# Optimization experiments

Hardware: AMD Instinct MI355X
Metric: run time of the kernel (lower is better)

The kernel has to match this reference:

```python
import jax, jax.numpy as jnp
import numpy as np

DIM = 64
WIDTH = 128
INPUT_DIM = 16
N_NODES = 50000
N_EDGES = 100000
N_GRAPHS = 2500
STEPS = 5


def setup_inputs() -> dict:
    key = jax.random.key(0)
    ks = jax.random.split(key, 24)
    d = DIM
    def nrm(i, shape, fan_in):
        return jax.random.normal(ks[i], shape, jnp.float32) / np.float32(np.sqrt(fan_in))
    return {
        "x": jax.random.normal(ks[0], (N_NODES, INPUT_DIM - 1), jnp.float32),
        "z": jax.random.normal(ks[1], (N_NODES,), jnp.float32),
        "edge_attr": jax.random.uniform(ks[2], (N_EDGES, 5), jnp.float32),
        "lin0_w": nrm(3, (INPUT_DIM, d), INPUT_DIM),
        "lin0_b": jnp.zeros((d,), jnp.float32),
        "emlp_w1": nrm(4, (5, WIDTH), 5),
        "emlp_b1": jnp.zeros((WIDTH,), jnp.float32),
        "emlp_w2": nrm(5, (WIDTH, d * d), WIDTH),
        "emlp_b2": jnp.zeros((d * d,), jnp.float32),
        "conv_root": nrm(6, (d, d), d),
        "conv_bias": jnp.zeros((d,), jnp.float32),
        "gru_wi": nrm(7, (3 * d, d), d),
        "gru_wh": nrm(8, (3 * d, d), d),
        "gru_bi": jnp.zeros((3 * d,), jnp.float32),
        "gru_bh": jnp.zeros((3 * d,), jnp.float32),
        "lstm_wi": nrm(9, (4 * d, 2 * d), 2 * d),
        "lstm_wh": nrm(10, (4 * d, d), d),
        "lstm_bi": jnp.zeros((4 * d,), jnp.float32),
        "lstm_bh": jnp.zeros((4 * d,), jnp.float32),
        "lin1_w": nrm(11, (2 * d, d), 2 * d),
        "lin1_b": jnp.zeros((d,), jnp.float32),
        "lin2_w": nrm(12, (d, 1), d),
        "lin2_b": jnp.zeros((1,), jnp.float32),
        "edge_index": jax.random.randint(ks[13], (2, N_EDGES), 0, N_NODES),
        "batch": jnp.sort(jax.random.randint(ks[14], (N_NODES,), 0, N_GRAPHS)),
        "num_graphs": N_GRAPHS,
    }


def reference(x, z, edge_attr, lin0_w, lin0_b, emlp_w1, emlp_b1, emlp_w2, emlp_b2,
              conv_root, conv_bias, gru_wi, gru_wh, gru_bi, gru_bh,
              lstm_wi, lstm_wh, lstm_bi, lstm_bh, lin1_w, lin1_b, lin2_w, lin2_b,
              edge_index, batch, num_graphs):
    d = lin0_w.shape[1]
    n = x.shape[0]
    src, dst = edge_index[0], edge_index[1]
    # lin0 on [x | z]
    out = jax.nn.relu(jnp.concatenate([x, z[:, None]], axis=-1) @ lin0_w + lin0_b)  # [N, d]
    h = out
    # edge MLP -> per-edge weight matrix [E, d, d] (edge_attr fixed, compute once)
    ew = (jax.nn.relu(edge_attr @ emlp_w1 + emlp_b1) @ emlp_w2 + emlp_b2).reshape(-1, d, d)
    deg = jax.ops.segment_sum(jnp.ones_like(src, jnp.float32), dst, num_segments=n)
    denom = jnp.maximum(deg, 1.0)[:, None]
    for _ in range(STEPS):
        # NNConv: gather-matmul-scatter(mean) + root transform + bias
        msg = jnp.einsum('ei,eio->eo', out[src], ew)  # [E, d]
        aggr = jax.ops.segment_sum(msg, dst, num_segments=n) / denom
        m = jax.nn.relu(aggr + out @ conv_root + conv_bias)
        # GRU cell (torch gate order r, z, n)
        gi = m @ gru_wi.T + gru_bi
        gh = h @ gru_wh.T + gru_bh
        i_r, i_z, i_n = jnp.split(gi, 3, axis=-1)
        h_r, h_z, h_n = jnp.split(gh, 3, axis=-1)
        r = jax.nn.sigmoid(i_r + h_r)
        zg = jax.nn.sigmoid(i_z + h_z)
        ng = jnp.tanh(i_n + r * h_n)
        h = (1.0 - zg) * ng + zg * h
        out = h
    # Set2Set pooling (LSTM(2d -> d), torch gate order i, f, g, o)
    B = num_graphs
    q_star = jnp.zeros((B, 2 * d), out.dtype)
    hh = jnp.zeros((B, d), out.dtype)
    cc = jnp.zeros((B, d), out.dtype)
    for _ in range(STEPS):
        g = q_star @ lstm_wi.T + lstm_bi + hh @ lstm_wh.T + lstm_bh
        gi_, gf_, gg_, go_ = jnp.split(g, 4, axis=-1)
        cc = jax.nn.sigmoid(gf_) * cc + jax.nn.sigmoid(gi_) * jnp.tanh(gg_)
        hh = jax.nn.sigmoid(go_) * jnp.tanh(cc)
        q = hh
        e = jnp.sum(out * q[batch], axis=-1)  # [N]
        emax = jax.ops.segment_max(e, batch, num_segments=B)
        a = jnp.exp(e - emax[batch])
        asum = jax.ops.segment_sum(a, batch, num_segments=B) + 1e-16
        a = a / asum[batch]
        r_pool = jax.ops.segment_sum(a[:, None] * out, batch, num_segments=B)  # [B, d]
        q_star = jnp.concatenate([q, r_pool], axis=-1)
    y = jax.nn.relu(q_star @ lin1_w + lin1_b) @ lin2_w + lin2_b
    return y.reshape(-1)
```

## Files before the change

kernel.cpp:

```cpp
#include <hip/hip_runtime.h>
#include <hip/hip_bf16.h>

#define NN 50000
#define NE 100000
#define NG 2500
#define WW 128
#define EPAD 100096
#define KCH 264

typedef _Float16 h8 __attribute__((ext_vector_type(8)));
typedef _Float16 h4 __attribute__((ext_vector_type(4)));
typedef float    f4 __attribute__((ext_vector_type(4)));

#define GLOAD_LDS16(g, l) __builtin_amdgcn_global_load_lds( \
    (const __attribute__((address_space(1))) void*)(g),     \
    (__attribute__((address_space(3))) void*)(l), 16, 0, 0)

__device__ __forceinline__ float sigf(float x) { return 1.0f / (1.0f + __expf(-x)); }

__global__ void k_zero4(float4* __restrict__ p, int n4) {
    int i = blockIdx.x * 256 + threadIdx.x;
    if (i < n4) p[i] = make_float4(0.f, 0.f, 0.f, 0.f);
}

__global__ void k_transpose(float* dst, const float* src, int rows, int cols) {
    int idx = blockIdx.x * 256 + threadIdx.x;
    if (idx >= rows * cols) return;
    int r = idx / cols, c = idx % cols;
    dst[c * rows + r] = src[idx];
}

__global__ void k_lin0(const float* __restrict__ x, const float* __restrict__ z,
                       const float* __restrict__ w, const float* __restrict__ b,
                       float* __restrict__ s, _Float16* __restrict__ s16) {
    int idx = blockIdx.x * 256 + threadIdx.x;
    int n = idx >> 6, o = idx & 63;
    float acc = b[o];
#pragma unroll
    for (int i = 0; i < 15; i++) acc += x[n * 15 + i] * w[i * 64 + o];
    acc += z[n] * w[15 * 64 + o];
    float r = fmaxf(acc, 0.0f);
    s[idx] = r;
    s16[idx] = (_Float16)r;
}

__global__ void k_deg(const int* __restrict__ dstI, float* __restrict__ deg) {
    int e = blockIdx.x * 256 + threadIdx.x;
    if (e < NE) atomicAdd(&deg[dstI[e]], 1.0f);
}

__global__ void k_gstart(const int* __restrict__ batch, int* __restrict__ gstart) {
    int n = blockIdx.x * 256 + threadIdx.x;
    if (n > NN) return;
    int b1 = (n < NN) ? batch[n] : NG;
    int b0 = (n == 0) ? -1 : batch[n - 1];
    for (int g = b0 + 1; g <= b1; g++) gstart[g] = n;
}

__global__ void k_emlp_t(const float* __restrict__ ea, const float* __restrict__ w1,
                         const float* __restrict__ b1, _Float16* __restrict__ hidT4) {
    __shared__ _Float16 hl[132][64];
    int t = threadIdx.x;
    int e0 = blockIdx.x * 64;
    int e_l = t & 63, w = t >> 6;
    int e = e0 + e_l;
    float a0 = 0, a1 = 0, a2 = 0, a3 = 0, a4 = 0;
    if (e < NE) {
        a0 = ea[e * 5 + 0]; a1 = ea[e * 5 + 1]; a2 = ea[e * 5 + 2];
        a3 = ea[e * 5 + 3]; a4 = ea[e * 5 + 4];
    }
    for (int h = w * 32; h < w * 32 + 32; h++) {
        float acc = b1[h];
        acc += a0 * w1[0 * 128 + h] + a1 * w1[1 * 128 + h] + a2 * w1[2 * 128 + h]
             + a3 * w1[3 * 128 + h] + a4 * w1[4 * 128 + h];
        hl[h][e_l] = (_Float16)fmaxf(acc, 0.0f);
    }
    if (t < 64) hl[128][t] = (_Float16)1.0f;
    else if (t < 128) hl[129][t - 64] = (_Float16)0.0f;
    else if (t < 192) hl[130][t - 128] = (_Float16)0.0f;
    else hl[131][t - 192] = (_Float16)0.0f;
    __syncthreads();
#pragma unroll
    for (int it = 0; it < 9; it++) {
        int hq = it * 4 + w;
        if (hq < 33) {
            h4 v = { hl[hq * 4 + 0][e_l], hl[hq * 4 + 1][e_l],
                     hl[hq * 4 + 2][e_l], hl[hq * 4 + 3][e_l] };
            *(h4*)(hidT4 + ((size_t)hq * EPAD + e0 + e_l) * 4) = v;
        }
    }
}

__global__ void k_prep_B(const float* __restrict__ w2, const float* __restrict__ b2,
                         _Float16* __restrict__ Bp) {
    int g = blockIdx.x * 256 + threadIdx.x;
    int l = g & 63, tt = (g >> 6) & 3, c = g >> 8;
    int n = tt * 16 + (l & 15);
    int kb = c * 32 + (l >> 4) * 8;
    h8 v;
#pragma unroll
    for (int j = 0; j < 8; j++) {
        int k = kb + j;
        float f = 0.0f;
        if (k < 8192) f = w2[(size_t)k * 64 + n];
        else if (k < 8256) f = b2[(k - 8192) * 64 + n];
        v[j] = (_Float16)f;
    }
    *((h8*)Bp + g) = v;
}

__global__ void k_prep_W(const float* __restrict__ conv_root,
                         const float* __restrict__ gru_wi,
                         const float* __restrict__ gru_wh,
                         _Float16* __restrict__ Bw) {
    int g = blockIdx.x * 256 + threadIdx.x;
    if (g >= 56 * 64) return;
    int l = g & 63, unit = g >> 6;
    int kb = ((unit & 1) * 32) + (l >> 4) * 8;
    h8 v;
    if (unit < 8) {
        int nt = unit >> 1;
        int n = nt * 16 + (l & 15);
#pragma unroll
        for (int j = 0; j < 8; j++) v[j] = (_Float16)conv_root[(kb + j) * 64 + n];
    } else if (unit < 32) {
        int nt = (unit - 8) >> 1;
        int o = nt * 16 + (l & 15);
#pragma unroll
        for (int j = 0; j < 8; j++) v[j] = (_Float16)gru_wi[o * 64 + kb + j];
    } else {
        int nt = (unit - 32) >> 1;
        int o = nt * 16 + (l & 15);
#pragma unroll
        for (int j = 0; j < 8; j++) v[j] = (_Float16)gru_wh[o * 64 + kb + j];
    }
    *((h8*)Bw + g) = v;
}

__global__ __launch_bounds__(256, 3) void k_fused(
        const _Float16* __restrict__ s16, const _Float16* __restrict__ hidT4,
        const _Float16* __restrict__ Bp, const int* __restrict__ srcI,
        const int* __restrict__ dstI, float* __restrict__ aggr) {
    __shared__ uint4 Bl[2][1024];
    int t = threadIdx.x, w = t >> 6, lane = t & 63;
    int m = lane & 15, q = lane >> 4;
    int ew0 = blockIdx.x * 256 + w * 64;

    h8 sA[4][2];
#pragma unroll
    for (int mt = 0; mt < 4; mt++) {
        int e = ew0 + mt * 16 + m;
        int src = (e < NE) ? srcI[e] : 0;
        const _Float16* sp = s16 + (size_t)src * 64;
        sA[mt][0] = *(const h8*)(sp + q * 8);
        sA[mt][1] = *(const h8*)(sp + 32 + q * 8);
    }
    f4 acc[4][4];
#pragma unroll
    for (int mt = 0; mt < 4; mt++)
#pragma unroll
        for (int nt = 0; nt < 4; nt++) acc[mt][nt] = (f4){0.f, 0.f, 0.f, 0.f};

    const h4* hT = (const h4*)hidT4;
    h4 hfA[4], hfB[4];
#pragma unroll
    for (int mt = 0; mt < 4; mt++)
        hfA[mt] = hT[(size_t)0 * EPAD + ew0 + mt * 16 + m];

    {
        const uint4* bs = (const uint4*)Bp;
#pragma unroll
        for (int r = 0; r < 4; r++) GLOAD_LDS16(bs + r * 256 + t, &Bl[0][r * 256 + t]);
    }
    __syncthreads();

#define COMPUTE_STEP(BUF, HH)                                                  \
    _Pragma("unroll")                                                          \
    for (int c2 = 0; c2 < 4; c2++) {                                           \
        h8 b0 = *(const h8*)&Bl[BUF][(c2 * 4 + 0) * 64 + lane];                \
        h8 b1 = *(const h8*)&Bl[BUF][(c2 * 4 + 1) * 64 + lane];                \
        h8 b2 = *(const h8*)&Bl[BUF][(c2 * 4 + 2) * 64 + lane];                \
        h8 b3 = *(const h8*)&Bl[BUF][(c2 * 4 + 3) * 64 + lane];                \
        _Pragma("unroll")                                                      \
        for (int mt = 0; mt < 4; mt++) {                                       \
            h8 a = sA[mt][c2 & 1] * hfA[mt][(HH) + (c2 >> 1)];                 \
            acc[mt][0] = __builtin_amdgcn_mfma_f32_16x16x32_f16(a, b0, acc[mt][0], 0, 0, 0); \
            acc[mt][1] = __builtin_amdgcn_mfma_f32_16x16x32_f16(a, b1, acc[mt][1], 0, 0, 0); \
            acc[mt][2] = __builtin_amdgcn_mfma_f32_16x16x32_f16(a, b2, acc[mt][2], 0, 0, 0); \
            acc[mt][3] = __builtin_amdgcn_mfma_f32_16x16x32_f16(a, b3, acc[mt][3], 0, 0, 0); \
        }                                                                      \
    }

    for (int tt = 0; tt < 33; tt++) {
        {
            const uint4* bs = (const uint4*)Bp + (size_t)(2 * tt + 1) * 1024;
#pragma unroll
            for (int r = 0; r < 4; r++) GLOAD_LDS16(bs + r * 256 + t, &Bl[1][r * 256 + t]);
        }
        {
#pragma unroll
            for (int mt = 0; mt < 4; mt++)
                hfB[mt] = hT[(size_t)(tt + 1) * EPAD + ew0 + mt * 16 + m];
        }
        COMPUTE_STEP(0, 0)
        __syncthreads();

        if (tt + 1 < 33) {
            const uint4* bs = (const uint4*)Bp + (size_t)(2 * tt + 2) * 1024;
#pragma unroll
            for (int r = 0; r < 4; r++) GLOAD_LDS16(bs + r * 256 + t, &Bl[0][r * 256 + t]);
        }
        COMPUTE_STEP(1, 2)
#pragma unroll
        for (int mt = 0; mt < 4; mt++) hfA[mt] = hfB[mt];
        __syncthreads();
    }
#undef COMPUTE_STEP

#pragma unroll
    for (int mt = 0; mt < 4; mt++) {
        int eb = ew0 + mt * 16 + q * 4;
#pragma unroll
        for (int r = 0; r < 4; r++) {
            int e = eb + r;
            if (e < NE) {
                int d = dstI[e];
                float* ap = aggr + (size_t)d * 64 + m;
                atomicAdd(ap + 0,  acc[mt][0][r]);
                atomicAdd(ap + 16, acc[mt][1][r]);
                atomicAdd(ap + 32, acc[mt][2][r]);
                atomicAdd(ap + 48, acc[mt][3][r]);
            }
        }
    }
}

__global__ __launch_bounds__(256) void k_combine2(
        float* __restrict__ s, _Float16* __restrict__ s16,
        float* __restrict__ aggr, const float* __restrict__ deg,
        const _Float16* __restrict__ Bw, const float* __restrict__ cb,
        const float* __restrict__ bi, const float* __restrict__ bh) {
    __shared__ _Float16 ml[4][16][72];
    int t = threadIdx.x, w = t >> 6, lane = t & 63;
    int m = lane & 15, q = lane >> 4;
    int nb = blockIdx.x * 64 + w * 16;

    h8 sa0, sa1;
    {
        int node = nb + m; if (node >= NN) node = NN - 1;
        const _Float16* sp = s16 + (size_t)node * 64;
        sa0 = *(const h8*)(sp + q * 8);
        sa1 = *(const h8*)(sp + 32 + q * 8);
    }
    const h8* BW = (const h8*)Bw;

    f4 X[4], GH[12];
#pragma unroll
    for (int nt = 0; nt < 4; nt++) {
        X[nt] = (f4){0.f, 0.f, 0.f, 0.f};
        X[nt] = __builtin_amdgcn_mfma_f32_16x16x32_f16(sa0, BW[(nt * 2 + 0) * 64 + lane], X[nt], 0, 0, 0);
        X[nt] = __builtin_amdgcn_mfma_f32_16x16x32_f16(sa1, BW[(nt * 2 + 1) * 64 + lane], X[nt], 0, 0, 0);
    }
#pragma unroll
    for (int nt = 0; nt < 12; nt++) {
        GH[nt] = (f4){0.f, 0.f, 0.f, 0.f};
        GH[nt] = __builtin_amdgcn_mfma_f32_16x16x32_f16(sa0, BW[(32 + nt * 2 + 0) * 64 + lane], GH[nt], 0, 0, 0);
        GH[nt] = __builtin_amdgcn_mfma_f32_16x16x32_f16(sa1, BW[(32 + nt * 2 + 1) * 64 + lane], GH[nt], 0, 0, 0);
    }
#pragma unroll
    for (int r = 0; r < 4; r++) {
        int node = nb + q * 4 + r;
        bool ok = node < NN;
        int nc = ok ? node : NN - 1;
        float dn = fmaxf(deg[nc], 1.0f);
#pragma unroll
        for (int nt = 0; nt < 4; nt++) {
            int o = nt * 16 + m;
            size_t ai = (size_t)nc * 64 + o;
            float av = aggr[ai];
            if (ok) aggr[ai] = 0.0f;
            float mv = X[nt][r] + av / dn + cb[o];
            ml[w][q * 4 + r][o] = (_Float16)fmaxf(mv, 0.0f);
        }
    }
    __syncthreads();
    h8 ma0 = *(const h8*)&ml[w][m][q * 8];
    h8 ma1 = *(const h8*)&ml[w][m][32 + q * 8];

    f4 GI[12];
#pragma unroll
    for (int nt = 0; nt < 12; nt++) {
        GI[nt] = (f4){0.f, 0.f, 0.f, 0.f};
        GI[nt] = __builtin_amdgcn_mfma_f32_16x16x32_f16(ma0, BW[(8 + nt * 2 + 0) * 64 + lane], GI[nt], 0, 0, 0);
        GI[nt] = __builtin_amdgcn_mfma_f32_16x16x32_f16(ma1, BW[(8 + nt * 2 + 1) * 64 + lane], GI[nt], 0, 0, 0);
    }
#pragma unroll
    for (int og = 0; og < 4; og++) {
        int o = og * 16 + m;
        float bir = bi[o],       bhr = bh[o];
        float biz = bi[64 + o],  bhz = bh[64 + o];
        float bin = bi[128 + o], bhn = bh[128 + o];
#pragma unroll
        for (int r = 0; r < 4; r++) {
            int node = nb + q * 4 + r;
            if (node >= NN) continue;
            float rr = sigf(GI[og][r] + bir + GH[og][r] + bhr);
            float zz = sigf(GI[4 + og][r] + biz + GH[4 + og][r] + bhz);
            float ng = tanhf(GI[8 + og][r] + bin + rr * (GH[8 + og][r] + bhn));
            float hold = s[(size_t)node * 64 + o];
            float hnew = (1.0f - zz) * ng + zz * hold;
            s[(size_t)node * 64 + o] = hnew;
            s16[(size_t)node * 64 + o] = (_Float16)hnew;
        }
    }
}

__global__ void k_s2s5(const float* __restrict__ LiT, const float* __restrict__ LhT,
                       const float* __restrict__ bi, const float* __restrict__ bh,
                       const float* __restrict__ s, const int* __restrict__ gstart,
                       float* __restrict__ e_v,
                       const float* __restrict__ w1, const float* __restrict__ b1,
                       const float* __restrict__ w2, const float* __restrict__ b2,
                       float* __restrict__ y) {
    __shared__ float qs[128], hv[64], cv[64], g[256], qn[64];
    int b = blockIdx.x, t = threadIdx.x;
    if (t < 128) qs[t] = 0.0f;
    if (t < 64) { hv[t] = 0.0f; cv[t] = 0.0f; }
    __syncthreads();
    int n0 = gstart[b], n1 = gstart[b + 1];

    for (int it = 0; it < 5; it++) {
        float acc = bi[t] + bh[t];
        for (int k = 0; k < 128; k++) acc += qs[k] * LiT[k * 256 + t];
        for (int k = 0; k < 64; k++) acc += hv[k] * LhT[k * 256 + t];
        g[t] = acc;
        __syncthreads();
        if (t < 64) {
            float c_new = sigf(g[64 + t]) * cv[t] + sigf(g[t]) * tanhf(g[128 + t]);
            cv[t] = c_new;
            float hq = sigf(g[192 + t]) * tanhf(c_new);
            hv[t] = hq;
            qn[t] = hq;
            qs[t] = hq;
            int o = t;
            float qv = qn[o];
            float mx = -3.4e38f;
            for (int n = n0; n < n1; n++) {
                float v = s[(size_t)n * 64 + o] * qv;
#pragma unroll
                for (int off = 32; off; off >>= 1) v += __shfl_xor(v, off, 64);
                if (o == 0) e_v[n] = v;
                mx = fmaxf(mx, v);
            }
            float asum = 0.0f, rp = 0.0f;
            for (int n = n0; n < n1; n++) {
                float a = __expf(e_v[n] - mx);
                asum += a;
                rp += a * s[(size_t)n * 64 + o];
            }
            qs[64 + o] = rp / (asum + 1e-16f);
        }
        __syncthreads();
    }

    if (t < 64) {
        float acc = b1[t];
        for (int k = 0; k < 128; k++) acc += qs[k] * w1[k * 64 + t];
        float hid = fmaxf(acc, 0.0f) * w2[t];
#pragma unroll
        for (int off = 32; off; off >>= 1) hid += __shfl_down(hid, off, 64);
        if (t == 0) y[b] = hid + b2[0];
    }
}

static inline void zero_f(float* p, size_t nfloats, hipStream_t stream) {
    int n4 = (int)(nfloats / 4);
    k_zero4<<<(n4 + 255) / 256, 256, 0, stream>>>((float4*)p, n4);
}

extern "C" void kernel_launch(void* const* d_in, const int* in_sizes, int n_in,
                              void* d_out, int out_size, void* d_ws, size_t ws_size,
                              hipStream_t stream) {
    const float* x       = (const float*)d_in[0];
    const float* z       = (const float*)d_in[1];
    const float* ea      = (const float*)d_in[2];
    const float* lin0_w  = (const float*)d_in[3];
    const float* lin0_b  = (const float*)d_in[4];
    const float* emlp_w1 = (const float*)d_in[5];
    const float* emlp_b1 = (const float*)d_in[6];
    const float* emlp_w2 = (const float*)d_in[7];
    const float* emlp_b2 = (const float*)d_in[8];
    const float* conv_r  = (const float*)d_in[9];
    const float* conv_b  = (const float*)d_in[10];
    const float* gru_wi  = (const float*)d_in[11];
    const float* gru_wh  = (const float*)d_in[12];
    const float* gru_bi  = (const float*)d_in[13];
    const float* gru_bh  = (const float*)d_in[14];
    const float* lstm_wi = (const float*)d_in[15];
    const float* lstm_wh = (const float*)d_in[16];
    const float* lstm_bi = (const float*)d_in[17];
    const float* lstm_bh = (const float*)d_in[18];
    const float* lin1_w  = (const float*)d_in[19];
    const float* lin1_b  = (const float*)d_in[20];
    const float* lin2_w  = (const float*)d_in[21];
    const float* lin2_b  = (const float*)d_in[22];
    const int* eidx      = (const int*)d_in[23];
    const int* batch     = (const int*)d_in[24];
    const int* srcI = eidx;
    const int* dstI = eidx + NE;
    float* y = (float*)d_out;

    char* w = (char*)d_ws;
    size_t off = 0;
    auto alloc = [&](size_t bytes) -> void* {
        void* p = w + off;
        off += (bytes + 255) & ~(size_t)255;
        return p;
    };
    float* s      = (float*)alloc((size_t)NN * 64 * 4);
    float* aggr   = (float*)alloc((size_t)NN * 64 * 4);
    float* deg    = (float*)alloc((size_t)NN * 4);
    float* e_v    = (float*)alloc((size_t)NN * 4);
    float* LiT    = (float*)alloc(256 * 128 * 4);
    float* LhT    = (float*)alloc(256 * 64 * 4);
    int*   gstart = (int*)alloc((size_t)(NG + 1) * 4);
    _Float16* s16 = (_Float16*)alloc((size_t)NN * 64 * 2);
    _Float16* hidT= (_Float16*)alloc((size_t)34 * EPAD * 4 * 2);
    _Float16* Bp  = (_Float16*)alloc((size_t)KCH * 4 * 64 * 8 * 2);
    _Float16* Bw  = (_Float16*)alloc((size_t)56 * 64 * 8 * 2);
    (void)ws_size;

    k_transpose<<<(256 * 128 + 255) / 256, 256, 0, stream>>>(LiT, lstm_wi, 256, 128);
    k_transpose<<<(256 * 64 + 255) / 256, 256, 0, stream>>>(LhT, lstm_wh, 256, 64);
    k_prep_W<<<14, 256, 0, stream>>>(conv_r, gru_wi, gru_wh, Bw);

    k_lin0<<<NN * 64 / 256, 256, 0, stream>>>(x, z, lin0_w, lin0_b, s, s16);
    zero_f(deg, NN, stream);
    k_deg<<<(NE + 255) / 256, 256, 0, stream>>>(dstI, deg);
    k_gstart<<<(NN + 256) / 256, 256, 0, stream>>>(batch, gstart);
    k_emlp_t<<<EPAD / 64, 256, 0, stream>>>(ea, emlp_w1, emlp_b1, hidT);
    k_prep_B<<<KCH * 4 * 64 / 256, 256, 0, stream>>>(emlp_w2, emlp_b2, Bp);
    zero_f(aggr, (size_t)NN * 64, stream);

    for (int step = 0; step < 5; step++) {
        k_fused<<<EPAD / 256, 256, 0, stream>>>(s16, hidT, Bp, srcI, dstI, aggr);
        k_combine2<<<(NN + 63) / 64, 256, 0, stream>>>(s, s16, aggr, deg, Bw,
                                                       conv_b, gru_bi, gru_bh);
    }

    k_s2s5<<<NG, 256, 0, stream>>>(LiT, LhT, lstm_bi, lstm_bh, s, gstart, e_v,
                                   lin1_w, lin1_b, lin2_w, lin2_b, y);
}
```

Measured before the change: 1.070 ms.

## Batch four graphs per Set2Set block with LDS-staged node features and online softmax

The Set2Set kernel now handles four graphs per block, one wavefront per graph. Each LSTM weight load is shared across the four graphs' gate computations. Node features for the block's graphs are staged once into LDS when they fit in 160 rows, and attention uses a single-pass online softmax with per-lane dot products instead of a shuffle reduction per node. There is a global-memory fallback for oversized groups, and the larger LDS footprint may lower occupancy.

```diff
diff --git a/kernel.cpp b/kernel.cpp
--- a/kernel.cpp
+++ b/kernel.cpp
@@ -7,6 +7,8 @@
 #define WW 128
 #define EPAD 100096
 #define KCH 264
+#define GPB 4
+#define SCAP 160
 
 typedef _Float16 h8 __attribute__((ext_vector_type(8)));
 typedef _Float16 h4 __attribute__((ext_vector_type(4)));
@@ -315,61 +317,121 @@
     }
 }
 
-__global__ void k_s2s5(const float* __restrict__ LiT, const float* __restrict__ LhT,
-                       const float* __restrict__ bi, const float* __restrict__ bh,
-                       const float* __restrict__ s, const int* __restrict__ gstart,
-                       float* __restrict__ e_v,
-                       const float* __restrict__ w1, const float* __restrict__ b1,
-                       const float* __restrict__ w2, const float* __restrict__ b2,
-                       float* __restrict__ y) {
-    __shared__ float qs[128], hv[64], cv[64], g[256], qn[64];
-    int b = blockIdx.x, t = threadIdx.x;
-    if (t < 128) qs[t] = 0.0f;
-    if (t < 64) { hv[t] = 0.0f; cv[t] = 0.0f; }
+__global__ __launch_bounds__(256) void k_s2s5(
+        const float* __restrict__ LiT, const float* __restrict__ LhT,
+        const float* __restrict__ bi, const float* __restrict__ bh,
+        const float* __restrict__ s, const int* __restrict__ gstart,
+        float* __restrict__ e_v,
+        const float* __restrict__ w1, const float* __restrict__ b1,
+        const float* __restrict__ w2, const float* __restrict__ b2,
+        float* __restrict__ y) {
+    __shared__ float sl[SCAP][65];
+    __shared__ float qs[GPB][128], hv[GPB][64], cv[GPB][64], gg[GPB][256];
+    __shared__ int ginfo[GPB + 1];
+    int t = threadIdx.x, w = t >> 6, o = t & 63;
+    int g0 = blockIdx.x * GPB;
+    if (t <= GPB) ginfo[t] = gstart[g0 + t];
+    if (t < 128) {
+#pragma unroll
+        for (int gr = 0; gr < GPB; gr++) qs[gr][t] = 0.0f;
+    }
+    if (t < 64) {
+#pragma unroll
+        for (int gr = 0; gr < GPB; gr++) { hv[gr][t] = 0.0f; cv[gr][t] = 0.0f; }
+    }
     __syncthreads();
-    int n0 = gstart[b], n1 = gstart[b + 1];
+    int n00 = ginfo[0];
+    int cnt4 = ginfo[GPB] - n00;
+    bool staged = (cnt4 <= SCAP);
+    if (staged) {
+        for (int idx = t; idx < cnt4 * 16; idx += 256) {
+            int node = idx >> 4, c4 = (idx & 15) * 4;
+            float4 v = *(const float4*)&s[(size_t)(n00 + node) * 64 + c4];
+            sl[node][c4 + 0] = v.x; sl[node][c4 + 1] = v.y;
+            sl[node][c4 + 2] = v.z; sl[node][c4 + 3] = v.w;
+        }
+    }
+    __syncthreads();
+    int myn0 = ginfo[w] - n00, myn1 = ginfo[w + 1] - n00;
 
     for (int it = 0; it < 5; it++) {
-        float acc = bi[t] + bh[t];
-        for (int k = 0; k < 128; k++) acc += qs[k] * LiT[k * 256 + t];
-        for (int k = 0; k < 64; k++) acc += hv[k] * LhT[k * 256 + t];
-        g[t] = acc;
+        float a0 = bi[t] + bh[t], a1 = a0, a2 = a0, a3 = a0;
+        for (int k = 0; k < 128; k++) {
+            float wv = LiT[k * 256 + t];
+            a0 += qs[0][k] * wv; a1 += qs[1][k] * wv;
+            a2 += qs[2][k] * wv; a3 += qs[3][k] * wv;
+        }
+        for (int k = 0; k < 64; k++) {
+            float wv = LhT[k * 256 + t];
+            a0 += hv[0][k] * wv; a1 += hv[1][k] * wv;
+            a2 += hv[2][k] * wv; a3 += hv[3][k] * wv;
+        }
+        gg[0][t] = a0; gg[1][t] = a1; gg[2][t] = a2; gg[3][t] = a3;
         __syncthreads();
-        if (t < 64) {
-            float c_new = sigf(g[64 + t]) * cv[t] + sigf(g[t]) * tanhf(g[128 + t]);
-            cv[t] = c_new;
-            float hq = sigf(g[192 + t]) * tanhf(c_new);
-            hv[t] = hq;
-            qn[t] = hq;
-            qs[t] = hq;
-            int o = t;
-            float qv = qn[o];
-            float mx = -3.4e38f;
-            for (int n = n0; n < n1; n++) {
-                float v = s[(size_t)n * 64 + o] * qv;
-#pragma unroll
-                for (int off = 32; off; off >>= 1) v += __shfl_xor(v, off, 64);
-                if (o == 0) e_v[n] = v;
-                mx = fmaxf(mx, v);
+        {
+            float c_new = sigf(gg[w][64 + o]) * cv[w][o] + sigf(gg[w][o]) * tanhf(gg[w][128 + o]);
+            cv[w][o] = c_new;
+            float hq = sigf(gg[w][192 + o]) * tanhf(c_new);
+            hv[w][o] = hq;
+            qs[w][o] = hq;
+            float m = -3.4e38f, l = 0.0f, r = 0.0f;
+            if (staged) {
+                for (int c0 = myn0; c0 < myn1; c0 += 64) {
+                    int nn = myn1 - c0; if (nn > 64) nn = 64;
+                    float e = -3.4e38f;
+                    if (o < nn) {
+                        const float* row = &sl[c0 + o][0];
+                        float acc = 0.0f;
+                        for (int k = 0; k < 64; k++) acc += row[k] * qs[w][k];
+                        e = acc;
+                    }
+                    float cm = e;
+#pragma unroll
+                    for (int off = 32; off; off >>= 1) cm = fmaxf(cm, __shfl_xor(cm, off, 64));
+                    float mn = fmaxf(m, cm);
+                    float a = (o < nn) ? __expf(e - mn) : 0.0f;
+                    float csum = a;
+#pragma unroll
+                    for (int off = 32; off; off >>= 1) csum += __shfl_xor(csum, off, 64);
+                    float scale = (m > -3.0e38f) ? __expf(m - mn) : 0.0f;
+                    l = l * scale + csum;
+                    r = r * scale;
+                    for (int j = 0; j < nn; j++) {
+                        float aj = __shfl(a, j, 64);
+                        r += aj * sl[c0 + j][o];
+                    }
+                    m = mn;
+                }
+            } else {
+                int an0 = myn0 + n00, an1 = myn1 + n00;
+                float mx = -3.4e38f;
+                for (int n = an0; n < an1; n++) {
+                    float v = s[(size_t)n * 64 + o] * hq;
+#pragma unroll
+                    for (int off = 32; off; off >>= 1) v += __shfl_xor(v, off, 64);
+                    if (o == 0) e_v[n] = v;
+                    mx = fmaxf(mx, v);
+                }
+                float asum = 0.0f, rp = 0.0f;
+                for (int n = an0; n < an1; n++) {
+                    float a = __expf(e_v[n] - mx);
+                    asum += a;
+                    rp += a * s[(size_t)n * 64 + o];
+                }
+                l = asum; r = rp;
             }
-            float asum = 0.0f, rp = 0.0f;
-            for (int n = n0; n < n1; n++) {
-                float a = __expf(e_v[n] - mx);
-                asum += a;
-                rp += a * s[(size_t)n * 64 + o];
-            }
-            qs[64 + o] = rp / (asum + 1e-16f);
+            qs[w][64 + o] = r / (l + 1e-16f);
         }
         __syncthreads();
     }
 
-    if (t < 64) {
-        float acc = b1[t];
-        for (int k = 0; k < 128; k++) acc += qs[k] * w1[k * 64 + t];
-        float hid = fmaxf(acc, 0.0f) * w2[t];
+    {
+        float acc = b1[o];
+        for (int k = 0; k < 128; k++) acc += qs[w][k] * w1[k * 64 + o];
+        float hid = fmaxf(acc, 0.0f) * w2[o];
 #pragma unroll
         for (int off = 32; off; off >>= 1) hid += __shfl_down(hid, off, 64);
-        if (t == 0) y[b] = hid + b2[0];
+        if (o == 0) y[g0 + w] = hid + b2[0];
     }
 }
 
@@ -448,6 +510,6 @@
                                                        conv_b, gru_bi, gru_bh);
     }
 
-    k_s2s5<<<NG, 256, 0, stream>>>(LiT, LhT, lstm_bi, lstm_bh, s, gstart, e_v,
-                                   lin1_w, lin1_b, lin2_w, lin2_b, y);
-}
+    k_s2s5<<<NG / GPB, 256, 0, stream>>>(LiT, LhT, lstm_bi, lstm_bh, s, gstart, e_v,
+                                         lin1_w, lin1_b, lin2_w, lin2_b, y);
+}
```

After: 904.4 us. -15.5%, faster.
